# Performance work log

Hardware: AMD Instinct MI355X
Metric: run time of the kernel (lower is better)

The kernel has to match this reference:

```python
import jax, jax.numpy as jnp
import numpy as np

B, H, W, DM = 4, 64, 64, 96
DS, DC, K = 16, 3, 4
DI = DM            # expand = 1.0
DTR = 6            # ceil(96/16)


def setup_inputs() -> dict:
    key = jax.random.key(0)
    ks = jax.random.split(key, 12)
    s = 0.02
    # dt bias init exactly as MS2D.dt_init: dt ~ exp(U*(log(max)-log(min))+log(min)); inv softplus
    dt = jnp.exp(jax.random.uniform(ks[5], (K, DI)) * (np.log(0.1) - np.log(0.001)) + np.log(0.001))
    dt = jnp.clip(dt, 1e-4, None)
    inv_dt = dt + jnp.log(-jnp.expm1(-dt))
    A_logs = jnp.log(jnp.broadcast_to(jnp.arange(1, DS + 1, dtype=jnp.float32), (K, DI, DS)))
    return {
        "x": jax.random.normal(ks[0], (B, H, W, DM), jnp.float32),
        "in_proj_w": jax.random.normal(ks[1], (2 * DI, DM), jnp.float32) * s,
        "conv_w": jax.random.normal(ks[2], (DI, 1, DC, DC), jnp.float32) * s,
        "conv_b": jnp.zeros((DI,), jnp.float32),
        "x_proj_weight": jax.random.normal(ks[3], (K, DTR + 2 * DS, DI), jnp.float32) * s,
        "dt_projs_weight": jax.random.uniform(ks[4], (K, DI, DTR), minval=-1.0, maxval=1.0) * (DTR ** -0.5),
        "dt_projs_bias": inv_dt,
        "A_logs": A_logs,
        "Ds": jnp.ones((K, DI), jnp.float32),
        "out_norm_w": jnp.ones((DI,), jnp.float32),
        "out_norm_b": jnp.zeros((DI,), jnp.float32),
        "out_proj_w": jax.random.normal(ks[6], (DM, DI), jnp.float32) * s,
    }


def _ms2d(x, in_proj_w, conv_w, conv_b, x_proj_weight, dt_projs_weight,
          dt_projs_bias, A_logs, Ds, out_norm_w, out_norm_b, out_proj_w):
    Bb, Hh, Ww, _ = x.shape
    L = Hh * Ww
    # in_proj -> (x, z) gating split
    xz = x @ in_proj_w.T                      # (B,H,W,2*DI)
    xc, z = jnp.split(xz, 2, axis=-1)
    xc = jnp.transpose(xc, (0, 3, 1, 2))      # (B,DI,H,W)
    xc = jax.lax.conv_general_dilated(
        xc, conv_w, (1, 1), 'SAME', feature_group_count=xc.shape[1],
        dimension_numbers=('NCHW', 'OIHW', 'NCHW')) + conv_b[None, :, None, None]
    xc = jax.nn.silu(xc)
    d = xc.shape[1]
    # 4-directional scan sequences: hw, wh, and their reverses
    x_hw = xc.reshape(Bb, d, L)
    x_wh = jnp.transpose(xc, (0, 1, 3, 2)).reshape(Bb, d, L)
    x2 = jnp.stack([x_hw, x_wh], axis=1)          # (B,2,d,L)
    xs = jnp.concatenate([x2, jnp.flip(x2, axis=-1)], axis=1)  # (B,4,d,L)
    x_dbl = jnp.einsum('bkdl,kcd->bkcl', xs, x_proj_weight)
    dtr = dt_projs_weight.shape[2]
    n = A_logs.shape[2]
    dts, Bs, Cs = jnp.split(x_dbl, [dtr, dtr + n], axis=2)     # (B,4,r,L),(B,4,N,L),(B,4,N,L)
    dts = jnp.einsum('bkrl,kdr->bkdl', dts, dt_projs_weight)
    delta = jax.nn.softplus(dts + dt_projs_bias[None, :, :, None])  # (B,4,d,L)
    A = -jnp.exp(A_logs)                                        # (4,d,N)
    # time-major for scan
    u_t = jnp.moveaxis(xs, -1, 0)       # (L,B,4,d)
    dl_t = jnp.moveaxis(delta, -1, 0)
    B_t = jnp.moveaxis(Bs, -1, 0)       # (L,B,4,N)
    C_t = jnp.moveaxis(Cs, -1, 0)

    def step(h, inp):                   # h: (B,4,d,N)
        u, dl, b, c = inp
        dA = jnp.exp(dl[..., None] * A)
        h = h * dA + (dl * u)[..., None] * b[:, :, None, :]
        y = jnp.einsum('bkdn,bkn->bkd', h, c)
        return h, y

    h0 = jnp.zeros((Bb, 4, d, n), xs.dtype)
    _, ys = jax.lax.scan(step, h0, (u_t, dl_t, B_t, C_t))
    ys = jnp.moveaxis(ys, 0, -1)        # (B,4,d,L)
    ys = ys + Ds[None, :, :, None] * xs  # skip D*u
    inv_y = jnp.flip(ys[:, 2:4], axis=-1)

    def wh2hw(t):  # undo the (W,H) raster order
        return jnp.transpose(t.reshape(Bb, d, Ww, Hh), (0, 1, 3, 2)).reshape(Bb, d, L)

    y = ys[:, 0] + inv_y[:, 0] + wh2hw(ys[:, 1]) + wh2hw(inv_y[:, 1])
    y = jnp.transpose(y, (0, 2, 1)).reshape(Bb, Hh, Ww, d)
    mu = y.mean(-1, keepdims=True)
    var = y.var(-1, keepdims=True)
    y = (y - mu) / jnp.sqrt(var + 1e-5) * out_norm_w + out_norm_b
    y = y * jax.nn.silu(z)
    return y @ out_proj_w.T


def reference(x, in_proj_w, conv_w, conv_b, x_proj_weight, dt_projs_weight,
              dt_projs_bias, A_logs, Ds, out_norm_w, out_norm_b, out_proj_w):
    return _ms2d(x, in_proj_w, conv_w, conv_b, x_proj_weight, dt_projs_weight,
                 dt_projs_bias, A_logs, Ds, out_norm_w, out_norm_b, out_proj_w)
```

## Files before the change

### kernel.cpp

```cpp
#include <hip/hip_runtime.h>
#include <math.h>


#define LQ 4096
#define NCH 128
#define LCH 32

__device__ __forceinline__ float sigmoid_f(float x){ return 1.0f/(1.0f + __expf(-x)); }
__device__ __forceinline__ float silu_f(float x){ return x * sigmoid_f(x); }
__device__ __forceinline__ float softplus_f(float x){ return (x > 20.0f) ? x : __logf(1.0f + __expf(x)); }

__device__ __forceinline__ int pos_of(int k, int i){
  switch(k & 3){
    case 0: return i;
    case 1: return ((i & 63) << 6) | (i >> 6);
    case 2: return LQ - 1 - i;
    default: { int j = LQ - 1 - i; return ((j & 63) << 6) | (j >> 6); }
  }
}

__device__ __forceinline__ void pow8(float r, int nh, float* e){
  e[0]=r;
  e[1]=r*r;
  e[2]=e[1]*r;
  e[3]=e[1]*e[1];
  e[4]=e[3]*r;
  e[5]=e[3]*e[1];
  e[6]=e[3]*e[2];
  e[7]=e[3]*e[3];
  float m = nh ? e[7] : 1.0f;
  #pragma unroll
  for (int j=0;j<8;j++) e[j] *= m;
}

__global__ __launch_bounds__(256) void k_inproj(const float* __restrict__ x,
                                                const float* __restrict__ wproj,
                                                float* __restrict__ xc,
                                                float* __restrict__ zb){
  __shared__ float a_s[64*97];
  __shared__ float w_s[96*97];
  const int t = threadIdx.x;
  const int row0 = (blockIdx.x >> 1) * 64;
  const int ch = blockIdx.x & 1;
  for (int e = t*4; e < 64*96; e += 1024){
    float4 v = *(const float4*)(x + (size_t)row0*96 + e);
    int r = e/96, c = e%96;
    float* p = a_s + r*97 + c;
    p[0]=v.x; p[1]=v.y; p[2]=v.z; p[3]=v.w;
  }
  for (int e = t*4; e < 96*96; e += 1024){
    float4 v = *(const float4*)(wproj + (size_t)ch*96*96 + e);
    int r = e/96, c = e%96;
    float* p = w_s + r*97 + c;
    p[0]=v.x; p[1]=v.y; p[2]=v.z; p[3]=v.w;
  }
  __syncthreads();
  const int tr = t >> 5, tc = t & 31;
  float acc[8][3];
  #pragma unroll
  for (int i=0;i<8;i++){
    #pragma unroll
    for (int j=0;j<3;j++) acc[i][j]=0.f;
  }
  for (int kk=0; kk<96; kk++){
    float a[8], b[3];
    #pragma unroll
    for (int i=0;i<8;i++) a[i] = a_s[(tr*8+i)*97+kk];
    #pragma unroll
    for (int j=0;j<3;j++) b[j] = w_s[(tc*3+j)*97+kk];
    #pragma unroll
    for (int i=0;i<8;i++){
      #pragma unroll
      for (int j=0;j<3;j++) acc[i][j] += a[i]*b[j];
    }
  }
  float* dst = ch ? zb : xc;
  #pragma unroll
  for (int i=0;i<8;i++){
    int row = row0 + tr*8 + i;
    #pragma unroll
    for (int j=0;j<3;j++) dst[(size_t)row*96 + tc*3 + j] = acc[i][j];
  }
}

__global__ __launch_bounds__(256) void k_conv(const float* __restrict__ xc,
                                              const float* __restrict__ cw,
                                              const float* __restrict__ cb,
                                              float* __restrict__ u){
  int e = blockIdx.x*256 + threadIdx.x;
  int d0 = (e % 24) * 4;
  int p = e / 24;
  int w = p & 63, h = (p >> 6) & 63, b = p >> 12;
  float cwv[4][9];
  #pragma unroll
  for (int q=0;q<4;q++){
    #pragma unroll
    for (int tp=0;tp<9;tp++) cwv[q][tp] = cw[(d0+q)*9+tp];
  }
  float4 acc = make_float4(cb[d0], cb[d0+1], cb[d0+2], cb[d0+3]);
  #pragma unroll
  for (int kh=0; kh<3; kh++){
    int hh = h + kh - 1;
    if (hh < 0 || hh > 63) continue;
    #pragma unroll
    for (int kw=0; kw<3; kw++){
      int ww = w + kw - 1;
      if (ww < 0 || ww > 63) continue;
      float4 v = *(const float4*)(xc + ((size_t)((b<<12) + (hh<<6) + ww))*96 + d0);
      int tp = kh*3+kw;
      acc.x += v.x*cwv[0][tp]; acc.y += v.y*cwv[1][tp];
      acc.z += v.z*cwv[2][tp]; acc.w += v.w*cwv[3][tp];
    }
  }
  float4 o = make_float4(silu_f(acc.x), silu_f(acc.y), silu_f(acc.z), silu_f(acc.w));
  *(float4*)(u + (size_t)p*96 + d0) = o;
}

__global__ __launch_bounds__(128) void k_proj(const float* __restrict__ u,
                                              const float* __restrict__ xpw,
                                              float* __restrict__ dts,
                                              float* __restrict__ Bsb,
                                              float* __restrict__ Csb,
                                              float* __restrict__ us){
  __shared__ float u_s[64*97];
  __shared__ float w_s[40*97];
  const int t = threadIdx.x;
  const int blk = blockIdx.x;
  const int pt = blk & 63, k = (blk >> 6) & 3, b = blk >> 8;
  const int bk = b*4 + k;
  const int i0 = pt * 64;
  for (int e = t*4; e < 64*96; e += 512){
    int row = e/96, c = e%96;
    int p = pos_of(k, i0 + row);
    float4 v = *(const float4*)(u + ((size_t)((b<<12) + p))*96 + c);
    float* dst = u_s + row*97 + c;
    dst[0]=v.x; dst[1]=v.y; dst[2]=v.z; dst[3]=v.w;
    if (us) *(float4*)(us + ((size_t)((bk<<12) + i0 + row))*96 + c) = v;
  }
  for (int e = t*4; e < 40*96; e += 512){
    int r = e/96, c = e%96;
    float4 v = (r < 38) ? *(const float4*)(xpw + (k*38+r)*96 + c)
                        : make_float4(0,0,0,0);
    float* p = w_s + r*97 + c;
    p[0]=v.x; p[1]=v.y; p[2]=v.z; p[3]=v.w;
  }
  __syncthreads();
  const int posg = t & 15, cg = t >> 4;
  float acc[4][5];
  #pragma unroll
  for (int i=0;i<4;i++){
    #pragma unroll
    for (int j=0;j<5;j++) acc[i][j]=0.f;
  }
  for (int dd=0; dd<96; dd++){
    float uu[4], wv[5];
    #pragma unroll
    for (int i=0;i<4;i++) uu[i] = u_s[(posg*4+i)*97+dd];
    #pragma unroll
    for (int j=0;j<5;j++) wv[j] = w_s[(cg*5+j)*97+dd];
    #pragma unroll
    for (int i=0;i<4;i++){
      #pragma unroll
      for (int j=0;j<5;j++) acc[i][j] += uu[i]*wv[j];
    }
  }
  #pragma unroll
  for (int i=0;i<4;i++){
    int ii = i0 + posg*4 + i;
    int base = (bk<<12) + ii;
    #pragma unroll
    for (int j=0;j<5;j++){
      int c = cg*5 + j;
      float v = acc[i][j];
      if (c < 6)       dts[(size_t)base*6 + c] = v;
      else if (c < 22) Bsb[(size_t)base*16 + (c-6)] = v;
      else if (c < 38) Csb[(size_t)base*16 + (c-22)] = v;
    }
  }
}

__global__ __launch_bounds__(384) void k_scanA(const float* __restrict__ u,
                                               const float* __restrict__ us,
                                               const float* __restrict__ dts,
                                               const float* __restrict__ Bsb,
                                               const float* __restrict__ dtw_g,
                                               const float* __restrict__ dtb_g,
                                               const float* __restrict__ Alogs,
                                               float* __restrict__ S,
                                               float* __restrict__ sumd){
  const int t = threadIdx.x;
  const int c2 = t / 192;
  const int lane = t & 63;
  const int wv3 = (t % 192) >> 6;
  const int nh = (lane >> 5) & 1;
  const int d = wv3*32 + (lane & 31);
  const int blk = blockIdx.x;
  const int bk = blk >> 6;
  const int k = bk & 3, b = bk >> 2;
  const int chunk = ((blk & 63) << 1) | c2;
  const int ibase = chunk * LCH;
  float An[8];
  bool fast = true;
  #pragma unroll
  for (int j=0;j<8;j++){
    int n = nh*8 + j;
    An[j] = -__expf(Alogs[(k*96+d)*16+n]);
    fast = fast && (fabsf(An[j] + (float)(n+1)) < 1e-3f*(float)(n+1));
  }
  int wfast = __all(fast ? 1 : 0);
  float dtw[6];
  #pragma unroll
  for (int r=0;r<6;r++) dtw[r] = dtw_g[(k*96+d)*6+r];
  const float bias = dtb_g[k*96+d];
  const float* uptr; long ustep;
  if (us){ uptr = us + ((size_t)((bk<<12)+ibase))*96 + d; ustep = 96; }
  else {
    int pb = pos_of(k, ibase);
    int pstep = pos_of(k, ibase+1) - pb;
    uptr = u + ((size_t)((b<<12)+pb))*96 + d; ustep = (long)pstep*96;
  }
  const float2* dtp = (const float2*)(dts + ((size_t)((bk<<12)+ibase))*6);
  const float4* Bp = (const float4*)(Bsb + ((size_t)((bk<<12)+ibase))*16) + nh*2;
  float h[8];
  #pragma unroll
  for (int n=0;n<8;n++) h[n]=0.f;
  float sdelta = 0.f;
  if (wfast){
    #pragma unroll 4
    for (int il=0; il<LCH; il++){
      float uv = *uptr;
      float2 q0 = dtp[0], q1 = dtp[1], q2 = dtp[2];
      float accd = bias + dtw[0]*q0.x + dtw[1]*q0.y + dtw[2]*q1.x
                        + dtw[3]*q1.y + dtw[4]*q2.x + dtw[5]*q2.y;
      float t1 = __expf(accd);
      float r = 1.0f / (1.0f + t1);
      float delta = (accd > 20.f) ? accd : __logf(1.0f + t1);
      sdelta += delta;
      float du = delta * uv;
      float4 b0 = Bp[0], b1 = Bp[1];
      float Bv[8] = {b0.x,b0.y,b0.z,b0.w, b1.x,b1.y,b1.z,b1.w};
      float e[8];
      pow8(r, nh, e);
      #pragma unroll
      for (int n=0;n<8;n++) h[n] = h[n]*e[n] + du*Bv[n];
      uptr += ustep; dtp += 3; Bp += 4;
    }
  } else {
    #pragma unroll 2
    for (int il=0; il<LCH; il++){
      float uv = *uptr;
      float2 q0 = dtp[0], q1 = dtp[1], q2 = dtp[2];
      float accd = bias + dtw[0]*q0.x + dtw[1]*q0.y + dtw[2]*q1.x
                        + dtw[3]*q1.y + dtw[4]*q2.x + dtw[5]*q2.y;
      float delta = softplus_f(accd);
      sdelta += delta;
      float du = delta * uv;
      float4 b0 = Bp[0], b1 = Bp[1];
      float Bv[8] = {b0.x,b0.y,b0.z,b0.w, b1.x,b1.y,b1.z,b1.w};
      float e[8];
      #pragma unroll
      for (int n=0;n<8;n++) e[n] = __expf(delta*An[n]);
      #pragma unroll
      for (int n=0;n<8;n++) h[n] = h[n]*e[n] + du*Bv[n];
      uptr += ustep; dtp += 3; Bp += 4;
    }
  }
  const int sb = (bk*NCH + chunk)*96 + d;
  float4* Sp = (float4*)(S + (size_t)sb*16 + nh*8);
  Sp[0] = make_float4(h[0],h[1],h[2],h[3]);
  Sp[1] = make_float4(h[4],h[5],h[6],h[7]);
  if (nh == 0) sumd[sb] = sdelta;
}

__global__ __launch_bounds__(256) void k_scanB(float* __restrict__ S,
                                               const float* __restrict__ sumd,
                                               const float* __restrict__ Alogs,
                                               float* ){
  const int t = blockIdx.x*256 + threadIdx.x;
  const int n = t & 15;
  const int d = (t >> 4) % 96;
  const int bk = t / 1536;
  const int k = bk & 3;
  const float An = -__expf(Alogs[(k*96+d)*16+n]);
  float h = 0.f;
  for (int c=0;c<NCH;c++){
    const int sb = (bk*NCH + c)*96 + d;
    const size_t idx = (size_t)sb*16 + n;
    float sOld = S[idx];
    float P = __expf(An * sumd[sb]);
    S[idx] = h;
    h = h*P + sOld;
  }
}

__global__ __launch_bounds__(384) void k_scanC(const float* __restrict__ u,
                                               const float* __restrict__ us,
                                               const float* __restrict__ dts,
                                               const float* __restrict__ Bsb,
                                               const float* __restrict__ Csb,
                                               const float* __restrict__ dtw_g,
                                               const float* __restrict__ dtb_g,
                                               const float* __restrict__ Alogs,
                                               const float* __restrict__ h0buf,
                                               float* __restrict__ ys){
  const int t = threadIdx.x;
  const int c2 = t / 192;
  const int lane = t & 63;
  const int wv3 = (t % 192) >> 6;
  const int nh = (lane >> 5) & 1;
  const int d = wv3*32 + (lane & 31);
  const int blk = blockIdx.x;
  const int bk = blk >> 6;
  const int k = bk & 3, b = bk >> 2;
  const int chunk = ((blk & 63) << 1) | c2;
  const int ibase = chunk * LCH;
  float An[8];
  bool fast = true;
  #pragma unroll
  for (int j=0;j<8;j++){
    int n = nh*8 + j;
    An[j] = -__expf(Alogs[(k*96+d)*16+n]);
    fast = fast && (fabsf(An[j] + (float)(n+1)) < 1e-3f*(float)(n+1));
  }
  int wfast = __all(fast ? 1 : 0);
  float dtw[6];
  #pragma unroll
  for (int r=0;r<6;r++) dtw[r] = dtw_g[(k*96+d)*6+r];
  const float bias = dtb_g[k*96+d];
  const int pb = pos_of(k, ibase);
  const int pstep = pos_of(k, ibase+1) - pb;
  const float* uptr; long ustep;
  if (us){ uptr = us + ((size_t)((bk<<12)+ibase))*96 + d; ustep = 96; }
  else   { uptr = u + ((size_t)((b<<12)+pb))*96 + d; ustep = (long)pstep*96; }
  const float2* dtp = (const float2*)(dts + ((size_t)((bk<<12)+ibase))*6);
  const float4* Bp = (const float4*)(Bsb + ((size_t)((bk<<12)+ibase))*16) + nh*2;
  const float4* Cp = (const float4*)(Csb + ((size_t)((bk<<12)+ibase))*16) + nh*2;
  float* yp = ys + ((size_t)((bk<<12)+pb))*96 + d;
  const long ystep = (long)pstep*96;
  float h[8];
  const int sb = (bk*NCH + chunk)*96 + d;
  const float4* Hp = (const float4*)(h0buf + (size_t)sb*16 + nh*8);
  {
    float4 h0=Hp[0], h1=Hp[1];
    h[0]=h0.x;h[1]=h0.y;h[2]=h0.z;h[3]=h0.w;
    h[4]=h1.x;h[5]=h1.y;h[6]=h1.z;h[7]=h1.w;
  }
  if (wfast){
    #pragma unroll 4
    for (int il=0; il<LCH; il++){
      float uv = *uptr;
      float2 q0 = dtp[0], q1 = dtp[1], q2 = dtp[2];
      float accd = bias + dtw[0]*q0.x + dtw[1]*q0.y + dtw[2]*q1.x
                        + dtw[3]*q1.y + dtw[4]*q2.x + dtw[5]*q2.y;
      float t1 = __expf(accd);
      float r = 1.0f / (1.0f + t1);
      float delta = (accd > 20.f) ? accd : __logf(1.0f + t1);
      float du = delta * uv;
      float4 b0 = Bp[0], b1 = Bp[1];
      float4 c0 = Cp[0], c1 = Cp[1];
      float Bv[8] = {b0.x,b0.y,b0.z,b0.w, b1.x,b1.y,b1.z,b1.w};
      float Cv[8] = {c0.x,c0.y,c0.z,c0.w, c1.x,c1.y,c1.z,c1.w};
      float e[8];
      pow8(r, nh, e);
      float y8 = 0.f;
      #pragma unroll
      for (int n=0;n<8;n++){
        h[n] = h[n]*e[n] + du*Bv[n];
        y8 += h[n]*Cv[n];
      }
      float y = y8 + __shfl_xor(y8, 32, 64);
      if (nh == 0) yp[il*ystep] = y;
      uptr += ustep; dtp += 3; Bp += 4; Cp += 4;
    }
  } else {
    #pragma unroll 2
    for (int il=0; il<LCH; il++){
      float uv = *uptr;
      float2 q0 = dtp[0], q1 = dtp[1], q2 = dtp[2];
      float accd = bias + dtw[0]*q0.x + dtw[1]*q0.y + dtw[2]*q1.x
                        + dtw[3]*q1.y + dtw[4]*q2.x + dtw[5]*q2.y;
      float delta = softplus_f(accd);
      float du = delta * uv;
      float4 b0 = Bp[0], b1 = Bp[1];
      float4 c0 = Cp[0], c1 = Cp[1];
      float Bv[8] = {b0.x,b0.y,b0.z,b0.w, b1.x,b1.y,b1.z,b1.w};
      float Cv[8] = {c0.x,c0.y,c0.z,c0.w, c1.x,c1.y,c1.z,c1.w};
      float e[8];
      #pragma unroll
      for (int n=0;n<8;n++) e[n] = __expf(delta*An[n]);
      float y8 = 0.f;
      #pragma unroll
      for (int n=0;n<8;n++){
        h[n] = h[n]*e[n] + du*Bv[n];
        y8 += h[n]*Cv[n];
      }
      float y = y8 + __shfl_xor(y8, 32, 64);
      if (nh == 0) yp[il*ystep] = y;
      uptr += ustep; dtp += 3; Bp += 4; Cp += 4;
    }
  }
}

__global__ __launch_bounds__(256) void k_out(const float* __restrict__ ys,
                                             const float* __restrict__ ubuf,
                                             const float* __restrict__ Dsg,
                                             const float* __restrict__ zbuf,
                                             const float* __restrict__ nw,
                                             const float* __restrict__ nb,
                                             const float* __restrict__ wout,
                                             float* __restrict__ out){
  __shared__ float w_s[96*97];
  __shared__ float g_s[32*97];
  const int t = threadIdx.x;
  const int b = blockIdx.x >> 7;
  const int pt = blockIdx.x & 127;
  const int p0 = pt * 32;
  for (int e=t*4; e<96*96; e+=1024){
    float4 v = *(const float4*)(wout+e);
    int r=e/96, c=e%96;
    float* p = w_s + r*97 + c;
    p[0]=v.x; p[1]=v.y; p[2]=v.z; p[3]=v.w;
  }
  const int pos = t >> 3, lane8 = t & 7, d0 = lane8*12;
  const int p = p0 + pos;
  float yv[12];
  float s1=0.f, s2=0.f;
  #pragma unroll
  for (int i=0;i<12;i+=4){
    float4 a = make_float4(0,0,0,0);
    #pragma unroll
    for (int kk=0;kk<4;kk++){
      float4 v = *(const float4*)(ys + ((size_t)(((b*4+kk)<<12) + p))*96 + d0 + i);
      a.x+=v.x; a.y+=v.y; a.z+=v.z; a.w+=v.w;
    }
    float4 uv = *(const float4*)(ubuf + ((size_t)((b<<12)+p))*96 + d0 + i);
    #pragma unroll
    for (int q=0;q<4;q++){
      int dd = d0+i+q;
      float sD = Dsg[dd] + Dsg[96+dd] + Dsg[192+dd] + Dsg[288+dd];
      float uq = (q==0)?uv.x:(q==1)?uv.y:(q==2)?uv.z:uv.w;
      float* aq = (q==0)?&a.x:(q==1)?&a.y:(q==2)?&a.z:&a.w;
      *aq += sD * uq;
    }
    yv[i]=a.x; yv[i+1]=a.y; yv[i+2]=a.z; yv[i+3]=a.w;
    s1 += a.x+a.y+a.z+a.w;
    s2 += a.x*a.x + a.y*a.y + a.z*a.z + a.w*a.w;
  }
  #pragma unroll
  for (int m=1; m<8; m<<=1){
    s1 += __shfl_xor(s1, m, 64);
    s2 += __shfl_xor(s2, m, 64);
  }
  const float mu = s1 * (1.0f/96.0f);
  const float var = s2 * (1.0f/96.0f) - mu*mu;
  const float rstd = rsqrtf(var + 1e-5f);
  #pragma unroll
  for (int i=0;i<12;i+=4){
    float4 zv = *(const float4*)(zbuf + ((size_t)((b<<12)+p))*96 + d0 + i);
    float zz[4] = {zv.x,zv.y,zv.z,zv.w};
    #pragma unroll
    for (int q=0;q<4;q++){
      int d = d0+i+q;
      float yn = (yv[i+q]-mu)*rstd*nw[d] + nb[d];
      g_s[pos*97 + d] = yn * silu_f(zz[q]);
    }
  }
  __syncthreads();
  const int posg = t >> 5, mg = t & 31;
  float acc[4][3];
  #pragma unroll
  for (int i=0;i<4;i++){
    #pragma unroll
    for (int j=0;j<3;j++) acc[i][j]=0.f;
  }
  for (int dd=0; dd<96; dd++){
    float g4[4], w3[3];
    #pragma unroll
    for (int i=0;i<4;i++) g4[i] = g_s[(posg*4+i)*97+dd];
    #pragma unroll
    for (int j=0;j<3;j++) w3[j] = w_s[(mg*3+j)*97+dd];
    #pragma unroll
    for (int i=0;i<4;i++){
      #pragma unroll
      for (int j=0;j<3;j++) acc[i][j] += g4[i]*w3[j];
    }
  }
  #pragma unroll
  for (int i=0;i<4;i++){
    int prow = p0 + posg*4 + i;
    #pragma unroll
    for (int j=0;j<3;j++){
      out[((size_t)((b<<12)+prow))*96 + mg*3 + j] = acc[i][j];
    }
  }
}

extern "C" void kernel_launch(void* const* d_in, const int* in_sizes, int n_in,
                              void* d_out, int out_size, void* d_ws, size_t ws_size,
                              hipStream_t stream) {
  (void)in_sizes; (void)n_in; (void)out_size;
  const float* x   = (const float*)d_in[0];
  const float* ipw = (const float*)d_in[1];
  const float* cw  = (const float*)d_in[2];
  const float* cb  = (const float*)d_in[3];
  const float* xpw = (const float*)d_in[4];
  const float* dtw = (const float*)d_in[5];
  const float* dtb = (const float*)d_in[6];
  const float* alg = (const float*)d_in[7];
  const float* dsg = (const float*)d_in[8];
  const float* nw  = (const float*)d_in[9];
  const float* nb  = (const float*)d_in[10];
  const float* wo  = (const float*)d_in[11];
  float* out = (float*)d_out;

  float* w = (float*)d_ws;
  size_t off = 0;
  float* z_b    = w + off; off += 1572864;
  float* u_b    = w + off; off += 1572864;
  float* dts_b  = w + off; off += 393216;
  float* Bs_b   = w + off; off += 1048576;
  float* Cs_b   = w + off; off += 1048576;
  float* Sh_b   = w + off; off += 3145728;
  float* sumd_b = w + off; off += 98304;
  float* ys_b   = w + off; off += 6291456;
  float* xc_b   = ys_b;
  size_t need_us = (off + 6291456) * sizeof(float);
  float* us_b = (ws_size >= need_us) ? (w + off) : nullptr;

  k_inproj<<<512, 256, 0, stream>>>(x, ipw, xc_b, z_b);
  k_conv  <<<1536, 256, 0, stream>>>(xc_b, cw, cb, u_b);
  k_proj  <<<1024, 128, 0, stream>>>(u_b, xpw, dts_b, Bs_b, Cs_b, us_b);
  k_scanA <<<1024, 384, 0, stream>>>(u_b, us_b, dts_b, Bs_b, dtw, dtb, alg, Sh_b, sumd_b);
  k_scanB <<<96, 256, 0, stream>>>(Sh_b, sumd_b, alg, nullptr);
  k_scanC <<<1024, 384, 0, stream>>>(u_b, us_b, dts_b, Bs_b, Cs_b, dtw, dtb, alg, Sh_b, ys_b);
  k_out   <<<512, 256, 0, stream>>>(ys_b, u_b, dsg, z_b, nw, nb, wo, out);
}
```

Measured before the change: 241.4 us.

## Replace chunk-scan replay with local-output plus state-correction pass and parallel carry scan

The first scan pass now emits chunk-local outputs (zero initial state) and cumulative delta, overwriting the scan-ordered u buffer in place. A new lightweight kernel then adds the carried-in state contribution C·(exp(A·cumdelta)·h0) per position, so the second full recurrence over the chunk is no longer replayed. The sequential 128-step cross-chunk carry kernel becomes a block-parallel Hillis-Steele scan in shared memory. Outputs stay in scan order and k_out gathers with permuted indices. The cost is extra memory traffic for the cumulative delta and the correction pass, plus more workspace.

```diff
diff --git a/kernel.cpp b/kernel.cpp
--- a/kernel.cpp
+++ b/kernel.cpp
@@ -20,14 +20,8 @@
 }
 
 __device__ __forceinline__ void pow8(float r, int nh, float* e){
-  e[0]=r;
-  e[1]=r*r;
-  e[2]=e[1]*r;
-  e[3]=e[1]*e[1];
-  e[4]=e[3]*r;
-  e[5]=e[3]*e[1];
-  e[6]=e[3]*e[2];
-  e[7]=e[3]*e[3];
+  e[0]=r; e[1]=r*r; e[2]=e[1]*r; e[3]=e[1]*e[1];
+  e[4]=e[3]*r; e[5]=e[3]*e[1]; e[6]=e[3]*e[2]; e[7]=e[3]*e[3];
   float m = nh ? e[7] : 1.0f;
   #pragma unroll
   for (int j=0;j<8;j++) e[j] *= m;
@@ -179,15 +173,118 @@
   }
 }
 
-__global__ __launch_bounds__(384) void k_scanA(const float* __restrict__ u,
-                                               const float* __restrict__ us,
-                                               const float* __restrict__ dts,
-                                               const float* __restrict__ Bsb,
-                                               const float* __restrict__ dtw_g,
-                                               const float* __restrict__ dtb_g,
-                                               const float* __restrict__ Alogs,
-                                               float* __restrict__ S,
-                                               float* __restrict__ sumd){
+__global__ __launch_bounds__(384) void k_scanA2(float* us,
+                                                const float* __restrict__ dts,
+                                                const float* __restrict__ Bsb,
+                                                const float* __restrict__ Csb,
+                                                const float* __restrict__ dtw_g,
+                                                const float* __restrict__ dtb_g,
+                                                const float* __restrict__ Alogs,
+                                                float* __restrict__ S,
+                                                float* __restrict__ sumd,
+                                                float* __restrict__ ys){
+  const int t = threadIdx.x;
+  const int c2 = t / 192;
+  const int lane = t & 63;
+  const int wv3 = (t % 192) >> 6;
+  const int nh = (lane >> 5) & 1;
+  const int d = wv3*32 + (lane & 31);
+  const int blk = blockIdx.x;
+  const int bk = blk >> 6;
+  const int k = bk & 3;
+  const int chunk = ((blk & 63) << 1) | c2;
+  const int ibase = chunk * LCH;
+  float An[8];
+  bool fast = true;
+  #pragma unroll
+  for (int j=0;j<8;j++){
+    int n = nh*8 + j;
+    An[j] = -__expf(Alogs[(k*96+d)*16+n]);
+    fast = fast && (fabsf(An[j] + (float)(n+1)) < 1e-3f*(float)(n+1));
+  }
+  int wfast = __all(fast ? 1 : 0);
+  float dtw[6];
+  #pragma unroll
+  for (int r=0;r<6;r++) dtw[r] = dtw_g[(k*96+d)*6+r];
+  const float bias = dtb_g[k*96+d];
+  float* usp = us + ((size_t)((bk<<12)+ibase))*96 + d;
+  const float2* dtp = (const float2*)(dts + ((size_t)((bk<<12)+ibase))*6);
+  const float4* Bp = (const float4*)(Bsb + ((size_t)((bk<<12)+ibase))*16) + nh*2;
+  const float4* Cp = (const float4*)(Csb + ((size_t)((bk<<12)+ibase))*16) + nh*2;
+  float* yp = ys + ((size_t)((bk<<12)+ibase))*96 + d;
+  float h[8];
+  #pragma unroll
+  for (int n=0;n<8;n++) h[n]=0.f;
+  float cum = 0.f;
+  if (wfast){
+    #pragma unroll 8
+    for (int il=0; il<LCH; il++){
+      float uv = usp[(size_t)il*96];
+      float2 q0 = dtp[il*3+0], q1 = dtp[il*3+1], q2 = dtp[il*3+2];
+      float accd = bias + dtw[0]*q0.x + dtw[1]*q0.y + dtw[2]*q1.x
+                        + dtw[3]*q1.y + dtw[4]*q2.x + dtw[5]*q2.y;
+      float t1 = __expf(accd);
+      float r = 1.0f / (1.0f + t1);
+      float delta = (accd > 20.f) ? accd : __logf(1.0f + t1);
+      cum += delta;
+      float du = delta * uv;
+      float4 b0 = Bp[il*4+0], b1 = Bp[il*4+1];
+      float4 c0 = Cp[il*4+0], c1 = Cp[il*4+1];
+      float Bv[8] = {b0.x,b0.y,b0.z,b0.w, b1.x,b1.y,b1.z,b1.w};
+      float Cv[8] = {c0.x,c0.y,c0.z,c0.w, c1.x,c1.y,c1.z,c1.w};
+      float e[8];
+      pow8(r, nh, e);
+      float y8 = 0.f;
+      #pragma unroll
+      for (int n=0;n<8;n++){
+        h[n] = h[n]*e[n] + du*Bv[n];
+        y8 += h[n]*Cv[n];
+      }
+      float y = y8 + __shfl_xor(y8, 32, 64);
+      if (nh == 0){ yp[(size_t)il*96] = y; usp[(size_t)il*96] = cum; }
+    }
+  } else {
+    #pragma unroll 2
+    for (int il=0; il<LCH; il++){
+      float uv = usp[(size_t)il*96];
+      float2 q0 = dtp[il*3+0], q1 = dtp[il*3+1], q2 = dtp[il*3+2];
+      float accd = bias + dtw[0]*q0.x + dtw[1]*q0.y + dtw[2]*q1.x
+                        + dtw[3]*q1.y + dtw[4]*q2.x + dtw[5]*q2.y;
+      float delta = softplus_f(accd);
+      cum += delta;
+      float du = delta * uv;
+      float4 b0 = Bp[il*4+0], b1 = Bp[il*4+1];
+      float4 c0 = Cp[il*4+0], c1 = Cp[il*4+1];
+      float Bv[8] = {b0.x,b0.y,b0.z,b0.w, b1.x,b1.y,b1.z,b1.w};
+      float Cv[8] = {c0.x,c0.y,c0.z,c0.w, c1.x,c1.y,c1.z,c1.w};
+      float e[8];
+      #pragma unroll
+      for (int n=0;n<8;n++) e[n] = __expf(delta*An[n]);
+      float y8 = 0.f;
+      #pragma unroll
+      for (int n=0;n<8;n++){
+        h[n] = h[n]*e[n] + du*Bv[n];
+        y8 += h[n]*Cv[n];
+      }
+      float y = y8 + __shfl_xor(y8, 32, 64);
+      if (nh == 0){ yp[(size_t)il*96] = y; usp[(size_t)il*96] = cum; }
+    }
+  }
+  const int sb = (bk*NCH + chunk)*96 + d;
+  float4* Sp = (float4*)(S + (size_t)sb*16 + nh*8);
+  Sp[0] = make_float4(h[0],h[1],h[2],h[3]);
+  Sp[1] = make_float4(h[4],h[5],h[6],h[7]);
+  if (nh == 0) sumd[sb] = cum;
+}
+
+__global__ __launch_bounds__(384) void k_scanA_fb(const float* __restrict__ u,
+                                                  const float* __restrict__ dts,
+                                                  const float* __restrict__ Bsb,
+                                                  const float* __restrict__ dtw_g,
+                                                  const float* __restrict__ dtb_g,
+                                                  const float* __restrict__ Alogs,
+                                                  float* __restrict__ S,
+                                                  float* __restrict__ sumd){
   const int t = threadIdx.x;
   const int c2 = t / 192;
   const int lane = t & 63;
@@ -212,58 +309,38 @@
   #pragma unroll
   for (int r=0;r<6;r++) dtw[r] = dtw_g[(k*96+d)*6+r];
   const float bias = dtb_g[k*96+d];
-  const float* uptr; long ustep;
-  if (us){ uptr = us + ((size_t)((bk<<12)+ibase))*96 + d; ustep = 96; }
-  else {
-    int pb = pos_of(k, ibase);
-    int pstep = pos_of(k, ibase+1) - pb;
-    uptr = u + ((size_t)((b<<12)+pb))*96 + d; ustep = (long)pstep*96;
-  }
+  int pb = pos_of(k, ibase);
+  int pstep = pos_of(k, ibase+1) - pb;
+  const float* uptr = u + ((size_t)((b<<12)+pb))*96 + d;
+  const long ustep = (long)pstep*96;
   const float2* dtp = (const float2*)(dts + ((size_t)((bk<<12)+ibase))*6);
   const float4* Bp = (const float4*)(Bsb + ((size_t)((bk<<12)+ibase))*16) + nh*2;
   float h[8];
   #pragma unroll
   for (int n=0;n<8;n++) h[n]=0.f;
   float sdelta = 0.f;
-  if (wfast){
-    #pragma unroll 4
-    for (int il=0; il<LCH; il++){
-      float uv = *uptr;
-      float2 q0 = dtp[0], q1 = dtp[1], q2 = dtp[2];
-      float accd = bias + dtw[0]*q0.x + dtw[1]*q0.y + dtw[2]*q1.x
-                        + dtw[3]*q1.y + dtw[4]*q2.x + dtw[5]*q2.y;
-      float t1 = __expf(accd);
-      float r = 1.0f / (1.0f + t1);
-      float delta = (accd > 20.f) ? accd : __logf(1.0f + t1);
-      sdelta += delta;
-      float du = delta * uv;
-      float4 b0 = Bp[0], b1 = Bp[1];
-      float Bv[8] = {b0.x,b0.y,b0.z,b0.w, b1.x,b1.y,b1.z,b1.w};
-      float e[8];
-      pow8(r, nh, e);
-      #pragma unroll
-      for (int n=0;n<8;n++) h[n] = h[n]*e[n] + du*Bv[n];
-      uptr += ustep; dtp += 3; Bp += 4;
-    }
-  } else {
-    #pragma unroll 2
-    for (int il=0; il<LCH; il++){
-      float uv = *uptr;
-      float2 q0 = dtp[0], q1 = dtp[1], q2 = dtp[2];
-      float accd = bias + dtw[0]*q0.x + dtw[1]*q0.y + dtw[2]*q1.x
-                        + dtw[3]*q1.y + dtw[4]*q2.x + dtw[5]*q2.y;
-      float delta = softplus_f(accd);
-      sdelta += delta;
-      float du = delta * uv;
-      float4 b0 = Bp[0], b1 = Bp[1];
-      float Bv[8] = {b0.x,b0.y,b0.z,b0.w, b1.x,b1.y,b1.z,b1.w};
-      float e[8];
+  #pragma unroll 4
+  for (int il=0; il<LCH; il++){
+    float uv = *uptr;
+    float2 q0 = dtp[0], q1 = dtp[1], q2 = dtp[2];
+    float accd = bias + dtw[0]*q0.x + dtw[1]*q0.y + dtw[2]*q1.x
+                      + dtw[3]*q1.y + dtw[4]*q2.x + dtw[5]*q2.y;
+    float t1 = __expf(accd);
+    float r = 1.0f / (1.0f + t1);
+    float delta = (accd > 20.f) ? accd : __logf(1.0f + t1);
+    sdelta += delta;
+    float du = delta * uv;
+    float4 b0 = Bp[0], b1 = Bp[1];
+    float Bv[8] = {b0.x,b0.y,b0.z,b0.w, b1.x,b1.y,b1.z,b1.w};
+    float e[8];
+    if (wfast){ pow8(r, nh, e); }
+    else {
       #pragma unroll
       for (int n=0;n<8;n++) e[n] = __expf(delta*An[n]);
-      #pragma unroll
-      for (int n=0;n<8;n++) h[n] = h[n]*e[n] + du*Bv[n];
-      uptr += ustep; dtp += 3; Bp += 4;
-    }
+    }
+    #pragma unroll
+    for (int n=0;n<8;n++) h[n] = h[n]*e[n] + du*Bv[n];
+    uptr += ustep; dtp += 3; Bp += 4;
   }
   const int sb = (bk*NCH + chunk)*96 + d;
   float4* Sp = (float4*)(S + (size_t)sb*16 + nh*8);
@@ -272,37 +349,146 @@
   if (nh == 0) sumd[sb] = sdelta;
 }
 
-__global__ __launch_bounds__(256) void k_scanB(float* __restrict__ S,
-                                               const float* __restrict__ sumd,
-                                               const float* __restrict__ Alogs,
-                                               float* ){
-  const int t = blockIdx.x*256 + threadIdx.x;
-  const int n = t & 15;
-  const int d = (t >> 4) % 96;
-  const int bk = t / 1536;
+__global__ __launch_bounds__(128) void k_scanB2(float* __restrict__ S,
+                                                const float* __restrict__ sumd,
+                                                const float* __restrict__ Alogs){
+  __shared__ float As[128*17];
+  __shared__ float Bs[128*17];
+  const int c = threadIdx.x;
+  const int blk = blockIdx.x;
+  const int d = blk % 96;
+  const int bk = blk / 96;
   const int k = bk & 3;
-  const float An = -__expf(Alogs[(k*96+d)*16+n]);
-  float h = 0.f;
-  for (int c=0;c<NCH;c++){
-    const int sb = (bk*NCH + c)*96 + d;
-    const size_t idx = (size_t)sb*16 + n;
-    float sOld = S[idx];
-    float P = __expf(An * sumd[sb]);
-    S[idx] = h;
-    h = h*P + sOld;
-  }
-}
-
-__global__ __launch_bounds__(384) void k_scanC(const float* __restrict__ u,
-                                               const float* __restrict__ us,
-                                               const float* __restrict__ dts,
-                                               const float* __restrict__ Bsb,
+  const int sb = (bk*NCH + c)*96 + d;
+  float a[16], bvals[16];
+  {
+    const float4* Sp = (const float4*)(S + (size_t)sb*16);
+    float4 s0=Sp[0], s1=Sp[1], s2=Sp[2], s3=Sp[3];
+    bvals[0]=s0.x;bvals[1]=s0.y;bvals[2]=s0.z;bvals[3]=s0.w;
+    bvals[4]=s1.x;bvals[5]=s1.y;bvals[6]=s1.z;bvals[7]=s1.w;
+    bvals[8]=s2.x;bvals[9]=s2.y;bvals[10]=s2.z;bvals[11]=s2.w;
+    bvals[12]=s3.x;bvals[13]=s3.y;bvals[14]=s3.z;bvals[15]=s3.w;
+  }
+  const float sd = sumd[sb];
+  bool fast = true;
+  float An[16];
+  #pragma unroll
+  for (int n=0;n<16;n++){
+    An[n] = -__expf(Alogs[(k*96+d)*16+n]);
+    fast = fast && (fabsf(An[n] + (float)(n+1)) < 1e-3f*(float)(n+1));
+  }
+  if (fast){
+    float q = __expf(-sd);
+    float p = q;
+    #pragma unroll
+    for (int n=0;n<16;n++){ a[n] = p; p *= q; }
+  } else {
+    #pragma unroll
+    for (int n=0;n<16;n++) a[n] = __expf(An[n]*sd);
+  }
+  #pragma unroll
+  for (int n=0;n<16;n++){ As[c*17+n] = a[n]; Bs[c*17+n] = bvals[n]; }
+  for (int dist=1; dist<128; dist<<=1){
+    __syncthreads();
+    float aL[16], bL[16];
+    if (c >= dist){
+      #pragma unroll
+      for (int n=0;n<16;n++){ aL[n] = As[(c-dist)*17+n]; bL[n] = Bs[(c-dist)*17+n]; }
+    }
+    __syncthreads();
+    if (c >= dist){
+      #pragma unroll
+      for (int n=0;n<16;n++){
+        bvals[n] = bL[n]*a[n] + bvals[n];
+        a[n] = aL[n]*a[n];
+        As[c*17+n] = a[n]; Bs[c*17+n] = bvals[n];
+      }
+    }
+  }
+  __syncthreads();
+  float h0[16];
+  #pragma unroll
+  for (int n=0;n<16;n++) h0[n] = (c == 0) ? 0.f : Bs[(c-1)*17+n];
+  float4* Sp = (float4*)(S + (size_t)sb*16);
+  Sp[0] = make_float4(h0[0],h0[1],h0[2],h0[3]);
+  Sp[1] = make_float4(h0[4],h0[5],h0[6],h0[7]);
+  Sp[2] = make_float4(h0[8],h0[9],h0[10],h0[11]);
+  Sp[3] = make_float4(h0[12],h0[13],h0[14],h0[15]);
+}
+
+__global__ __launch_bounds__(256) void k_scanY(const float* __restrict__ us,
                                                const float* __restrict__ Csb,
-                                               const float* __restrict__ dtw_g,
-                                               const float* __restrict__ dtb_g,
                                                const float* __restrict__ Alogs,
                                                const float* __restrict__ h0buf,
                                                float* __restrict__ ys){
+  const int t = threadIdx.x;
+  const int blk = blockIdx.x;
+  const int dslice = blk % 3;
+  const int tmp = blk / 3;
+  const int chunk = tmp & 127;
+  const int bk = tmp >> 7;
+  const int k = bk & 3;
+  const int il = t >> 3;
+  const int d0 = ((t & 7) + dslice*8) * 4;
+  const int i = chunk*LCH + il;
+  const size_t rowb = (size_t)((bk<<12) + i);
+  float4 cd = *(const float4*)(us + rowb*96 + d0);
+  float4 yl = *(const float4*)(ys + rowb*96 + d0);
+  float Cv[16];
+  {
+    const float4* Cp = (const float4*)(Csb + rowb*16);
+    float4 c0=Cp[0], c1=Cp[1], c2=Cp[2], c3=Cp[3];
+    Cv[0]=c0.x;Cv[1]=c0.y;Cv[2]=c0.z;Cv[3]=c0.w;
+    Cv[4]=c1.x;Cv[5]=c1.y;Cv[6]=c1.z;Cv[7]=c1.w;
+    Cv[8]=c2.x;Cv[9]=c2.y;Cv[10]=c2.z;Cv[11]=c2.w;
+    Cv[12]=c3.x;Cv[13]=c3.y;Cv[14]=c3.z;Cv[15]=c3.w;
+  }
+  float yout[4] = {yl.x, yl.y, yl.z, yl.w};
+  float cdv[4] = {cd.x, cd.y, cd.z, cd.w};
+  #pragma unroll
+  for (int dd=0; dd<4; dd++){
+    const int d = d0 + dd;
+    const int sb = (bk*NCH + chunk)*96 + d;
+    float h0[16];
+    {
+      const float4* Hp = (const float4*)(h0buf + (size_t)sb*16);
+      float4 h0a=Hp[0], h1a=Hp[1], h2a=Hp[2], h3a=Hp[3];
+      h0[0]=h0a.x;h0[1]=h0a.y;h0[2]=h0a.z;h0[3]=h0a.w;
+      h0[4]=h1a.x;h0[5]=h1a.y;h0[6]=h1a.z;h0[7]=h1a.w;
+      h0[8]=h2a.x;h0[9]=h2a.y;h0[10]=h2a.z;h0[11]=h2a.w;
+      h0[12]=h3a.x;h0[13]=h3a.y;h0[14]=h3a.z;h0[15]=h3a.w;
+    }
+    bool fast = true;
+    float An[16];
+    #pragma unroll
+    for (int n=0;n<16;n++){
+      An[n] = -__expf(Alogs[(k*96+d)*16+n]);
+      fast = fast && (fabsf(An[n] + (float)(n+1)) < 1e-3f*(float)(n+1));
+    }
+    float acc = 0.f;
+    if (fast){
+      float q = __expf(-cdv[dd]);
+      float p = q;
+      #pragma unroll
+      for (int n=0;n<16;n++){ acc += Cv[n]*h0[n]*p; p *= q; }
+    } else {
+      #pragma unroll
+      for (int n=0;n<16;n++) acc += Cv[n]*h0[n]*__expf(An[n]*cdv[dd]);
+    }
+    yout[dd] += acc;
+  }
+  *(float4*)(ys + rowb*96 + d0) = make_float4(yout[0], yout[1], yout[2], yout[3]);
+}
+
+__global__ __launch_bounds__(384) void k_scanC_fb(const float* __restrict__ u,
+                                                  const float* __restrict__ dts,
+                                                  const float* __restrict__ Bsb,
+                                                  const float* __restrict__ Csb,
+                                                  const float* __restrict__ dtw_g,
+                                                  const float* __restrict__ dtb_g,
+                                                  const float* __restrict__ Alogs,
+                                                  const float* __restrict__ h0buf,
+                                                  float* __restrict__ ys){
   const int t = threadIdx.x;
   const int c2 = t / 192;
   const int lane = t & 63;
@@ -327,16 +513,14 @@
   #pragma unroll
   for (int r=0;r<6;r++) dtw[r] = dtw_g[(k*96+d)*6+r];
   const float bias = dtb_g[k*96+d];
-  const int pb = pos_of(k, ibase);
-  const int pstep = pos_of(k, ibase+1) - pb;
-  const float* uptr; long ustep;
-  if (us){ uptr = us + ((size_t)((bk<<12)+ibase))*96 + d; ustep = 96; }
-  else   { uptr = u + ((size_t)((b<<12)+pb))*96 + d; ustep = (long)pstep*96; }
+  int pb = pos_of(k, ibase);
+  int pstep = pos_of(k, ibase+1) - pb;
+  const float* uptr = u + ((size_t)((b<<12)+pb))*96 + d;
+  const long ustep = (long)pstep*96;
   const float2* dtp = (const float2*)(dts + ((size_t)((bk<<12)+ibase))*6);
   const float4* Bp = (const float4*)(Bsb + ((size_t)((bk<<12)+ibase))*16) + nh*2;
   const float4* Cp = (const float4*)(Csb + ((size_t)((bk<<12)+ibase))*16) + nh*2;
-  float* yp = ys + ((size_t)((bk<<12)+pb))*96 + d;
-  const long ystep = (long)pstep*96;
+  float* yp = ys + ((size_t)((bk<<12)+ibase))*96 + d;
   float h[8];
   const int sb = (bk*NCH + chunk)*96 + d;
   const float4* Hp = (const float4*)(h0buf + (size_t)sb*16 + nh*8);
@@ -345,59 +529,35 @@
     h[0]=h0.x;h[1]=h0.y;h[2]=h0.z;h[3]=h0.w;
     h[4]=h1.x;h[5]=h1.y;h[6]=h1.z;h[7]=h1.w;
   }
-  if (wfast){
-    #pragma unroll 4
-    for (int il=0; il<LCH; il++){
-      float uv = *uptr;
-      float2 q0 = dtp[0], q1 = dtp[1], q2 = dtp[2];
-      float accd = bias + dtw[0]*q0.x + dtw[1]*q0.y + dtw[2]*q1.x
-                        + dtw[3]*q1.y + dtw[4]*q2.x + dtw[5]*q2.y;
-      float t1 = __expf(accd);
-      float r = 1.0f / (1.0f + t1);
-      float delta = (accd > 20.f) ? accd : __logf(1.0f + t1);
-      float du = delta * uv;
-      float4 b0 = Bp[0], b1 = Bp[1];
-      float4 c0 = Cp[0], c1 = Cp[1];
-      float Bv[8] = {b0.x,b0.y,b0.z,b0.w, b1.x,b1.y,b1.z,b1.w};
-      float Cv[8] = {c0.x,c0.y,c0.z,c0.w, c1.x,c1.y,c1.z,c1.w};
-      float e[8];
-      pow8(r, nh, e);
-      float y8 = 0.f;
-      #pragma unroll
-      for (int n=0;n<8;n++){
-        h[n] = h[n]*e[n] + du*Bv[n];
-        y8 += h[n]*Cv[n];
-      }
-      float y = y8 + __shfl_xor(y8, 32, 64);
-      if (nh == 0) yp[il*ystep] = y;
-      uptr += ustep; dtp += 3; Bp += 4; Cp += 4;
-    }
-  } else {
-    #pragma unroll 2
-    for (int il=0; il<LCH; il++){
-      float uv = *uptr;
-      float2 q0 = dtp[0], q1 = dtp[1], q2 = dtp[2];
-      float accd = bias + dtw[0]*q0.x + dtw[1]*q0.y + dtw[2]*q1.x
-                        + dtw[3]*q1.y + dtw[4]*q2.x + dtw[5]*q2.y;
-      float delta = softplus_f(accd);
-      float du = delta * uv;
-      float4 b0 = Bp[0], b1 = Bp[1];
-      float4 c0 = Cp[0], c1 = Cp[1];
-      float Bv[8] = {b0.x,b0.y,b0.z,b0.w, b1.x,b1.y,b1.z,b1.w};
-      float Cv[8] = {c0.x,c0.y,c0.z,c0.w, c1.x,c1.y,c1.z,c1.w};
-      float e[8];
+  #pragma unroll 4
+  for (int il=0; il<LCH; il++){
+    float uv = *uptr;
+    float2 q0 = dtp[0], q1 = dtp[1], q2 = dtp[2];
+    float accd = bias + dtw[0]*q0.x + dtw[1]*q0.y + dtw[2]*q1.x
+                      + dtw[3]*q1.y + dtw[4]*q2.x + dtw[5]*q2.y;
+    float t1 = __expf(accd);
+    float r = 1.0f / (1.0f + t1);
+    float delta = (accd > 20.f) ? accd : __logf(1.0f + t1);
+    float du = delta * uv;
+    float4 b0 = Bp[0], b1 = Bp[1];
+    float4 c0 = Cp[0], c1 = Cp[1];
+    float Bv[8] = {b0.x,b0.y,b0.z,b0.w, b1.x,b1.y,b1.z,b1.w};
+    float Cv[8] = {c0.x,c0.y,c0.z,c0.w, c1.x,c1.y,c1.z,c1.w};
+    float e[8];
+    if (wfast){ pow8(r, nh, e); }
+    else {
       #pragma unroll
       for (int n=0;n<8;n++) e[n] = __expf(delta*An[n]);
-      float y8 = 0.f;
-      #pragma unroll
-      for (int n=0;n<8;n++){
-        h[n] = h[n]*e[n] + du*Bv[n];
-        y8 += h[n]*Cv[n];
-      }
-      float y = y8 + __shfl_xor(y8, 32, 64);
-      if (nh == 0) yp[il*ystep] = y;
-      uptr += ustep; dtp += 3; Bp += 4; Cp += 4;
-    }
+    }
+    float y8 = 0.f;
+    #pragma unroll
+    for (int n=0;n<8;n++){
+      h[n] = h[n]*e[n] + du*Bv[n];
+      y8 += h[n]*Cv[n];
+    }
+    float y = y8 + __shfl_xor(y8, 32, 64);
+    if (nh == 0) yp[(size_t)il*96] = y;
+    uptr += ustep; dtp += 3; Bp += 4; Cp += 4;
   }
 }
 
@@ -423,6 +583,9 @@
   }
   const int pos = t >> 3, lane8 = t & 7, d0 = lane8*12;
   const int p = p0 + pos;
+  const int tp = ((p & 63) << 6) | (p >> 6);
+  int idx[4];
+  idx[0] = p; idx[1] = tp; idx[2] = LQ-1-p; idx[3] = LQ-1-tp;
   float yv[12];
   float s1=0.f, s2=0.f;
   #pragma unroll
@@ -430,7 +593,7 @@
     float4 a = make_float4(0,0,0,0);
     #pragma unroll
     for (int kk=0;kk<4;kk++){
-      float4 v = *(const float4*)(ys + ((size_t)(((b*4+kk)<<12) + p))*96 + d0 + i);
+      float4 v = *(const float4*)(ys + ((size_t)(((b*4+kk)<<12) + idx[kk]))*96 + d0 + i);
       a.x+=v.x; a.y+=v.y; a.z+=v.z; a.w+=v.w;
     }
     float4 uv = *(const float4*)(ubuf + ((size_t)((b<<12)+p))*96 + d0 + i);
@@ -521,17 +684,26 @@
   float* Bs_b   = w + off; off += 1048576;
   float* Cs_b   = w + off; off += 1048576;
   float* Sh_b   = w + off; off += 3145728;
-  float* sumd_b = w + off; off += 98304;
   float* ys_b   = w + off; off += 6291456;
   float* xc_b   = ys_b;
-  size_t need_us = (off + 6291456) * sizeof(float);
-  float* us_b = (ws_size >= need_us) ? (w + off) : nullptr;
+  size_t need_primary = (off + 196608 + 6291456) * sizeof(float);
+  float* sumd_ded = w + off;
+  float* us_b     = w + off + 196608;
+  bool primary = (ws_size >= need_primary);
+  float* sumd_b = primary ? sumd_ded : ys_b;
 
   k_inproj<<<512, 256, 0, stream>>>(x, ipw, xc_b, z_b);
   k_conv  <<<1536, 256, 0, stream>>>(xc_b, cw, cb, u_b);
-  k_proj  <<<1024, 128, 0, stream>>>(u_b, xpw, dts_b, Bs_b, Cs_b, us_b);
-  k_scanA <<<1024, 384, 0, stream>>>(u_b, us_b, dts_b, Bs_b, dtw, dtb, alg, Sh_b, sumd_b);
-  k_scanB <<<96, 256, 0, stream>>>(Sh_b, sumd_b, alg, nullptr);
-  k_scanC <<<1024, 384, 0, stream>>>(u_b, us_b, dts_b, Bs_b, Cs_b, dtw, dtb, alg, Sh_b, ys_b);
+  k_proj  <<<1024, 128, 0, stream>>>(u_b, xpw, dts_b, Bs_b, Cs_b, primary ? us_b : nullptr);
+  if (primary){
+    k_scanA2<<<1024, 384, 0, stream>>>(us_b, dts_b, Bs_b, Cs_b, dtw, dtb, alg,
+                                       Sh_b, sumd_b, ys_b);
+    k_scanB2<<<1536, 128, 0, stream>>>(Sh_b, sumd_b, alg);
+    k_scanY <<<6144, 256, 0, stream>>>(us_b, Cs_b, alg, Sh_b, ys_b);
+  } else {
+    k_scanA_fb<<<1024, 384, 0, stream>>>(u_b, dts_b, Bs_b, dtw, dtb, alg, Sh_b, sumd_b);
+    k_scanB2<<<1536, 128, 0, stream>>>(Sh_b, sumd_b, alg);
+    k_scanC_fb<<<1024, 384, 0, stream>>>(u_b, dts_b, Bs_b, Cs_b, dtw, dtb, alg, Sh_b, ys_b);
+  }
   k_out   <<<512, 256, 0, stream>>>(ys_b, u_b, dsg, z_b, nw, nb, wo, out);
 }
```

Measured after the change: 301.0 us. +24.7%, slower.
